# Kernel tuning notes

Measured on AMD Instinct MI355X. Metric: run time of the kernel, lower is better.

The kernel has to match this reference:

```python
import jax, jax.numpy as jnp
import numpy as np

NUM_EXPERTS = 8
TOP_K = 2
HIDDEN = 1024
INTER = 4096
B, S = 4, 2048


def setup_inputs() -> dict:
    key = jax.random.key(0)
    ks = jax.random.split(key, 5)
    scale_h = 1.0 / np.sqrt(HIDDEN)
    scale_f = 1.0 / np.sqrt(INTER)
    return {
        "hidden_states": jax.random.normal(ks[0], (B, S, HIDDEN), dtype=jnp.float32),
        "router_w": jax.random.normal(ks[1], (HIDDEN, NUM_EXPERTS), dtype=jnp.float32) * scale_h,
        "gate_w": jax.random.normal(ks[2], (NUM_EXPERTS, HIDDEN, INTER), dtype=jnp.float32) * scale_h,
        "up_w": jax.random.normal(ks[3], (NUM_EXPERTS, HIDDEN, INTER), dtype=jnp.float32) * scale_h,
        "down_w": jax.random.normal(ks[4], (NUM_EXPERTS, INTER, HIDDEN), dtype=jnp.float32) * scale_f,
    }


def reference(hidden_states, router_w, gate_w, up_w, down_w):
    # hidden_states: [B, S, D]
    Bsz, Sl, D = hidden_states.shape
    E = gate_w.shape[0]

    router_logits = jnp.einsum("bsd,de->bse", hidden_states, router_w)
    router_probs = jax.nn.softmax(router_logits, axis=-1)          # [B,S,E]
    expert_weights, expert_indices = jax.lax.top_k(router_probs, TOP_K)  # [B,S,K]
    expert_weights = expert_weights / jnp.sum(expert_weights, axis=-1, keepdims=True)

    # load-balance loss: usage_e = count(idx==e)/num_tokens (sums to K)
    num_tokens = Bsz * Sl
    one_hot = jax.nn.one_hot(expert_indices, E, dtype=router_probs.dtype)  # [B,S,K,E]
    expert_usage = jnp.sum(one_hot, axis=(0, 1, 2)) / num_tokens           # [E]
    mean_routing_prob = jnp.mean(router_probs, axis=(0, 1))                # [E]
    load_balance_loss = jnp.sum(expert_usage * mean_routing_prob) * E

    # combine weight per token per expert: [B,S,E]
    combine_w = jnp.einsum("bsk,bske->bse", expert_weights, one_hot)

    output = jnp.zeros_like(hidden_states)
    for e in range(E):  # small fixed expert count
        gate = jax.nn.silu(jnp.einsum("bsd,df->bsf", hidden_states, gate_w[e]))
        up = jnp.einsum("bsd,df->bsf", hidden_states, up_w[e])
        expert_out = jnp.einsum("bsf,fd->bsd", gate * up, down_w[e])
        output = output + combine_w[..., e, None] * expert_out

    return output, load_balance_loss
```

## Files before the change

### kernel.cpp

```cpp
#include <hip/hip_runtime.h>
#include <stdint.h>

#define T_TOK 8192
#define D_HID 1024
#define F_INT 4096
#define NEXP 8
#define NT2 (T_TOK*2)
#define BMR 256
#define NTIL 72
#define CBANKS 64

typedef __attribute__((ext_vector_type(4))) float f32x4;
typedef __attribute__((ext_vector_type(8))) __bf16 bf16x8;
typedef unsigned short u16;

__device__ __forceinline__ unsigned short f2bf(float x) {
  unsigned int u = __float_as_uint(x);
  u = u + 0x7FFFu + ((u >> 16) & 1u);
  return (unsigned short)(u >> 16);
}
__device__ __forceinline__ void gload_lds16(const void* g, void* l) {
  __builtin_amdgcn_global_load_lds(
      (const __attribute__((address_space(1))) unsigned int*)g,
      (__attribute__((address_space(3))) unsigned int*)l, 16, 0, 0);
}
__device__ __forceinline__ void wait_vm8() {
  asm volatile("s_waitcnt vmcnt(8)" ::: "memory");
  __builtin_amdgcn_sched_barrier(0);
}
__device__ __forceinline__ void wait_vm0() {
  asm volatile("s_waitcnt vmcnt(0)" ::: "memory");
  __builtin_amdgcn_sched_barrier(0);
}
__device__ __forceinline__ void wait_lgkm0() {
  asm volatile("s_waitcnt lgkmcnt(0)" ::: "memory");
  __builtin_amdgcn_sched_barrier(0);
}
__device__ __forceinline__ int tswz(int x) { return (x & 7) * 9 + (x >> 3); }

#define MFMA(a,b,c) __builtin_amdgcn_mfma_f32_16x16x32_bf16((a),(b),(c),0,0,0)

__global__ __launch_bounds__(256) void k_cvt_all(
    const float* __restrict__ gw, const float* __restrict__ uw,
    const float* __restrict__ dw,
    u16* __restrict__ gT, u16* __restrict__ uT, u16* __restrict__ dT) {
  int bx = blockIdx.x;
  int grp = bx >> 13;
  int idx = bx & 8191;
  int e = idx >> 10;
  int rem = idx & 1023;
  const float* in; u16* out; int R, C, cx, cy;
  if (grp == 0)      { in = gw; out = gT; R = D_HID; C = F_INT; cx = rem & 63; cy = rem >> 6; }
  else if (grp == 1) { in = uw; out = uT; R = D_HID; C = F_INT; cx = rem & 63; cy = rem >> 6; }
  else               { in = dw; out = dT; R = F_INT; C = D_HID; cx = rem & 15; cy = rem >> 4; }
  const size_t mat = (size_t)R * C;
  const float* ip = in + (size_t)e * mat;
  u16* op = out + (size_t)e * mat;
  int c0 = cx * 64, r0 = cy * 64;
  __shared__ float Tf[64][68];
  int t = threadIdx.x;
#pragma unroll
  for (int p = 0; p < 4; p++) {
    int r = p * 16 + (t >> 4);
    int c = (t & 15) * 4;
    float4 v = *(const float4*)(ip + (size_t)(r0 + r) * C + (c0 + c));
    *(float4*)&Tf[r][c] = v;
  }
  __syncthreads();
  int f = t >> 2, seg = (t & 3) * 16;
  union { u16 s[8]; uint4 q; } o0, o1;
#pragma unroll
  for (int j = 0; j < 8; j++) {
    o0.s[j] = f2bf(Tf[seg + j][f]);
    o1.s[j] = f2bf(Tf[seg + 8 + j][f]);
  }
  *(uint4*)(op + (size_t)(c0 + f) * R + r0 + seg) = o0.q;
  *(uint4*)(op + (size_t)(c0 + f) * R + r0 + seg + 8) = o1.q;
}

__global__ __launch_bounds__(256) void k_router(const float* __restrict__ h,
                                                const float* __restrict__ rw,
                                                u16* __restrict__ hb,
                                                int* __restrict__ cntB,
                                                float* __restrict__ psumB,
                                                int* __restrict__ topk_e,
                                                float* __restrict__ topk_w) {
  int t = blockIdx.x * 4 + (threadIdx.x >> 6);
  int l = threadIdx.x & 63;
  const float* hr = h + (size_t)t * D_HID;
  u16* hbr = hb + (size_t)t * D_HID;
  double acc[NEXP];
#pragma unroll
  for (int e = 0; e < NEXP; e++) acc[e] = 0.0;
#pragma unroll
  for (int it = 0; it < 4; it++) {
    int i = it * 256 + l * 4;
    float4 x4 = *(const float4*)(hr + i);
    union { u16 s[4]; uint2 q; } o;
    o.s[0] = f2bf(x4.x); o.s[1] = f2bf(x4.y); o.s[2] = f2bf(x4.z); o.s[3] = f2bf(x4.w);
    *(uint2*)(hbr + i) = o.q;
    const float* xp = &x4.x;
#pragma unroll
    for (int k = 0; k < 4; k++) {
      double x = (double)xp[k];
      const float4* r4 = (const float4*)(rw + (size_t)(i + k) * NEXP);
      float4 a = r4[0], b = r4[1];
      acc[0] += x * a.x; acc[1] += x * a.y; acc[2] += x * a.z; acc[3] += x * a.w;
      acc[4] += x * b.x; acc[5] += x * b.y; acc[6] += x * b.z; acc[7] += x * b.w;
    }
  }
#pragma unroll
  for (int m = 32; m >= 1; m >>= 1) {
#pragma unroll
    for (int e = 0; e < NEXP; e++) acc[e] += __shfl_xor(acc[e], m, 64);
  }
  if (l == 0) {
    double mx = acc[0];
#pragma unroll
    for (int e = 1; e < NEXP; e++) mx = fmax(mx, acc[e]);
    double p[NEXP], s = 0.0;
#pragma unroll
    for (int e = 0; e < NEXP; e++) { p[e] = exp(acc[e] - mx); s += p[e]; }
    int i0 = 0;
#pragma unroll
    for (int e = 1; e < NEXP; e++) if (p[e] > p[i0]) i0 = e;
    int i1 = (i0 == 0) ? 1 : 0;
#pragma unroll
    for (int e = 0; e < NEXP; e++) if (e != i0 && p[e] > p[i1]) i1 = e;
    double w0 = p[i0] / (p[i0] + p[i1]);
    topk_e[t] = i0 | (i1 << 8);
    topk_w[2 * t] = (float)w0;
    topk_w[2 * t + 1] = (float)(1.0 - w0);
    int bank = t & (CBANKS - 1);
    atomicAdd(&cntB[i0 * CBANKS + bank], 1);
    atomicAdd(&cntB[i1 * CBANKS + bank], 1);
    float inv = (float)(1.0 / s);
#pragma unroll
    for (int e = 0; e < NEXP; e++) atomicAdd(&psumB[e * CBANKS + bank], (float)p[e] * inv);
  }
}

__global__ void k_scan(const int* __restrict__ cntB, const float* __restrict__ psumB,
                       int* __restrict__ offs, int4* __restrict__ tiles,
                       int* __restrict__ meta, float* __restrict__ loss_out,
                       int* __restrict__ cnt2) {
  int l = threadIdx.x;
  int cs[NEXP]; float ps[NEXP];
#pragma unroll
  for (int e = 0; e < NEXP; e++) {
    int c = cntB[e * CBANKS + l];
    float p = psumB[e * CBANKS + l];
#pragma unroll
    for (int m = 32; m >= 1; m >>= 1) {
      c += __shfl_xor(c, m, 64);
      p += __shfl_xor(p, m, 64);
    }
    cs[e] = c; ps[e] = p;
  }
  if (l == 0) {
    int off = 0, tc = 0;
    double loss = 0.0;
    for (int e = 0; e < NEXP; e++) {
      loss += ((double)cs[e] / (double)T_TOK) * ((double)ps[e] / (double)T_TOK);
      offs[e] = off;
      int nt = (cs[e] + BMR - 1) / BMR;
      for (int j = 0; j < nt; j++) {
        int rem = cs[e] - j * BMR;
        tiles[tc] = make_int4(e, off + j * BMR, rem < BMR ? rem : BMR, 0);
        tc++;
      }
      off += cs[e];
      cnt2[e] = 0;
    }
    offs[NEXP] = off;
    meta[0] = tc;
    loss_out[0] = (float)(loss * (double)NEXP);
  }
}

__global__ __launch_bounds__(256) void k_scatter(const int* __restrict__ topk_e,
                                                 const float* __restrict__ topk_w,
                                                 const int* __restrict__ offs,
                                                 int* __restrict__ cnt2,
                                                 int* __restrict__ rowtok,
                                                 float* __restrict__ roww,
                                                 int* __restrict__ invmap) {
  int t = blockIdx.x * 256 + threadIdx.x;
  if (t >= T_TOK) return;
  int ee = topk_e[t];
#pragma unroll
  for (int k = 0; k < 2; k++) {
    int e = (ee >> (8 * k)) & 255;
    int pos = offs[e] + atomicAdd(&cnt2[e], 1);
    rowtok[pos] = t;
    roww[pos] = topk_w[2 * t + k];
    invmap[2 * t + k] = pos;
  }
}

__global__ __launch_bounds__(256) void k_combine(const float* __restrict__ P,
                                                 const int* __restrict__ invmap,
                                                 float* __restrict__ out) {
  int t = blockIdx.x;
  int d = threadIdx.x * 4;
  int pA = invmap[2 * t], pB = invmap[2 * t + 1];
  float4 a0 = *(const float4*)(P + (size_t)pA * D_HID + d);
  float4 a1 = *(const float4*)(P + ((size_t)NT2 + pA) * D_HID + d);
  float4 b0 = *(const float4*)(P + (size_t)pB * D_HID + d);
  float4 b1 = *(const float4*)(P + ((size_t)NT2 + pB) * D_HID + d);
  float4 r;
  r.x = (a0.x + a1.x) + (b0.x + b1.x);
  r.y = (a0.y + a1.y) + (b0.y + b1.y);
  r.z = (a0.z + a1.z) + (b0.z + b1.z);
  r.w = (a0.w + a1.w) + (b0.w + b1.w);
  *(float4*)(out + (size_t)t * D_HID + d) = r;
}

template <int MODE>
__global__ __launch_bounds__(512, 2) void k_mm8(
    const u16* __restrict__ Asrc, const u16* __restrict__ Bsrc,
    const u16* __restrict__ Bsrc2,
    const int4* __restrict__ tiles, const int* __restrict__ meta,
    const int* __restrict__ rowtok, const float* __restrict__ roww,
    u16* __restrict__ G, float* __restrict__ out,
    int fcb, int FC, int KLEN) {
  int bx, by;
  if constexpr (MODE == 3) {
    int s = ((int)blockIdx.x & 7) * 36 + ((int)blockIdx.x >> 3);
    bx = s >> 2; by = s & 3;
  } else {
    bx = tswz(blockIdx.x); by = blockIdx.y;
  }
  if (bx >= meta[0]) return;
  int4 td = tiles[bx];
  int eid = td.x, row0 = td.y, nrows = td.z;
  int kz = blockIdx.z;
  size_t kz_byte = (size_t)kz * KLEN * 2;

  __shared__ __align__(16) u16 lds[2][2][BMR][64];

  int tid = threadIdx.x;
  int l = tid & 63, wid = tid >> 6;
  int wr = wid >> 2, wc = wid & 3;

  int rr0 = wid * 8 + (l >> 3);
  int sw = ((l & 7) ^ (rr0 & 7)) << 4;
  const char* pA[4]; const char* pB[4];
#pragma unroll
  for (int j = 0; j < 4; j++) {
    int rr = j * 64 + rr0;
    if constexpr (MODE == 0) {
      int tok = rowtok[row0 + ((rr < nrows) ? rr : 0)];
      pA[j] = (const char*)Asrc + (size_t)tok * (D_HID * 2) + sw;
      const u16* wsrc = (j < 2) ? Bsrc : Bsrc2;
      int frow = fcb + by * 128 + (rr & 127);
      pB[j] = (const char*)wsrc + ((size_t)eid * F_INT + frow) * (D_HID * 2) + sw;
    } else {
      pA[j] = (const char*)Asrc + (size_t)(row0 + rr) * (FC * 2) + kz_byte + sw;
      int brow = by * 256 + rr;
      pB[j] = (const char*)Bsrc + ((size_t)eid * D_HID + brow) * (F_INT * 2) + kz_byte + sw;
    }
  }

  int ch0 = (((l >> 4) + 0) ^ (l & 7)) << 4;
  int ch1 = (((l >> 4) + 4) ^ (l & 7)) << 4;
  int offA = (wr * 128 + (l & 15)) * 128;
  int offBn[4];
#pragma unroll
  for (int n = 0; n < 4; n++) {
    int r;
    if constexpr (MODE == 0)
      r = (n < 2) ? (wc * 32 + n * 16) : (128 + wc * 32 + (n - 2) * 16);
    else
      r = wc * 64 + n * 16;
    offBn[n] = 32768 + (r + (l & 15)) * 128;
  }
  const char* base = (const char*)&lds[0][0][0][0];
#define LDA(b,m,s) (*(const bf16x8*)(base + (b)*65536 + offA + (m)*2048 + ((s)?ch1:ch0)))
#define LDB(b,n,s) (*(const bf16x8*)(base + (b)*65536 + offBn[n] + ((s)?ch1:ch0)))

  f32x4 acc[8][4];
#pragma unroll
  for (int m = 0; m < 8; m++)
#pragma unroll
    for (int n = 0; n < 4; n++) acc[m][n] = f32x4{0.f, 0.f, 0.f, 0.f};

  auto STAGE = [&](int b, int mat, const char* const* p, int kt) {
#pragma unroll
    for (int j = 0; j < 4; j++)
      gload_lds16(p[j] + (size_t)kt * 128, &lds[b][mat][j * 64 + wid * 8][0]);
  };

  auto TILE = [&](int b, int kts, bool dostage, int vm) {
    bf16x8 fa[4][2], fb[4][2];
#pragma unroll
    for (int m = 0; m < 4; m++) { fa[m][0] = LDA(b, m, 0); fa[m][1] = LDA(b, m, 1); }
#pragma unroll
    for (int n = 0; n < 2; n++) { fb[n][0] = LDB(b, n, 0); fb[n][1] = LDB(b, n, 1); }
    asm volatile("s_waitcnt lgkmcnt(8)" ::: "memory");
    __builtin_amdgcn_s_barrier();
    wait_lgkm0();
    __builtin_amdgcn_s_setprio(1);
#pragma unroll
    for (int m = 0; m < 4; m++)
#pragma unroll
      for (int n = 0; n < 2; n++) {
        acc[m][n] = MFMA(fa[m][0], fb[n][0], acc[m][n]);
        acc[m][n] = MFMA(fa[m][1], fb[n][1], acc[m][n]);
      }
    __builtin_amdgcn_s_setprio(0);
    __builtin_amdgcn_s_barrier();
#pragma unroll
    for (int n = 2; n < 4; n++) { fb[n][0] = LDB(b, n, 0); fb[n][1] = LDB(b, n, 1); }
    __builtin_amdgcn_s_barrier();
    wait_lgkm0();
    __builtin_amdgcn_s_setprio(1);
#pragma unroll
    for (int m = 0; m < 4; m++)
#pragma unroll
      for (int n = 2; n < 4; n++) {
        acc[m][n] = MFMA(fa[m][0], fb[n][0], acc[m][n]);
        acc[m][n] = MFMA(fa[m][1], fb[n][1], acc[m][n]);
      }
    __builtin_amdgcn_s_setprio(0);
    __builtin_amdgcn_s_barrier();
#pragma unroll
    for (int m = 0; m < 4; m++) { fa[m][0] = LDA(b, 4 + m, 0); fa[m][1] = LDA(b, 4 + m, 1); }
    if (dostage) STAGE(b, 1, pB, kts);
    __builtin_amdgcn_s_barrier();
    wait_lgkm0();
    __builtin_amdgcn_s_setprio(1);
#pragma unroll
    for (int m = 0; m < 4; m++)
#pragma unroll
      for (int n = 0; n < 2; n++) {
        acc[4 + m][n] = MFMA(fa[m][0], fb[n][0], acc[4 + m][n]);
        acc[4 + m][n] = MFMA(fa[m][1], fb[n][1], acc[4 + m][n]);
      }
    __builtin_amdgcn_s_setprio(0);
    __builtin_amdgcn_s_barrier();
    if (dostage) STAGE(b, 0, pA, kts);
    if (vm == 8) wait_vm8();
    else if (vm == 0) wait_vm0();
    __builtin_amdgcn_s_barrier();
    __builtin_amdgcn_s_setprio(1);
#pragma unroll
    for (int m = 0; m < 4; m++)
#pragma unroll
      for (int n = 2; n < 4; n++) {
        acc[4 + m][n] = MFMA(fa[m][0], fb[n][0], acc[4 + m][n]);
        acc[4 + m][n] = MFMA(fa[m][1], fb[n][1], acc[4 + m][n]);
      }
    __builtin_amdgcn_s_setprio(0);
    __builtin_amdgcn_s_barrier();
  };

  int NT = KLEN / 64;
  STAGE(0, 1, pB, 0); STAGE(0, 0, pA, 0);
  STAGE(1, 1, pB, 1); STAGE(1, 0, pA, 1);
  wait_vm8();
  __builtin_amdgcn_s_barrier();

  int NIT = NT / 2;
  for (int it = 0; it < NIT - 1; ++it) {
    TILE(0, 2 * it + 2, true, 8);
    TILE(1, 2 * it + 3, true, 8);
  }
  TILE(0, 0, false, 0);
  TILE(1, 0, false, -1);

  int lr = (l >> 4) * 4, lc = l & 15;
#pragma unroll
  for (int m = 0; m < 8; m++) {
    int rbase = wr * 128 + m * 16 + lr;
#pragma unroll
    for (int j = 0; j < 4; j++) {
      int r = rbase + j;
      if (r < nrows) {
        if constexpr (MODE == 0) {
          size_t gb = (size_t)(row0 + r) * FC + by * 128 + wc * 32 + lc;
#pragma unroll
          for (int n = 0; n < 2; n++) {
            float g = acc[m][n][j], u = acc[m][n + 2][j];
            float sv = g / (1.0f + __expf(-g));
            G[gb + n * 16] = f2bf(sv * u);
          }
        } else if constexpr (MODE == 2) {
          float w = roww[row0 + r];
          int tok = rowtok[row0 + r];
          size_t ob = (size_t)tok * D_HID + by * 256 + wc * 64 + lc;
#pragma unroll
          for (int n = 0; n < 4; n++) atomicAdd(&out[ob + n * 16], acc[m][n][j] * w);
        } else {
          float w = roww[row0 + r];
          size_t pb = ((size_t)kz * NT2 + (row0 + r)) * D_HID + by * 256 + wc * 64 + lc;
#pragma unroll
          for (int n = 0; n < 4; n++) out[pb + n * 16] = acc[m][n][j] * w;
        }
      }
    }
  }
#undef LDA
#undef LDB
}

extern "C" void kernel_launch(void* const* d_in, const int* in_sizes, int n_in,
                              void* d_out, int out_size, void* d_ws, size_t ws_size,
                              hipStream_t stream) {
  (void)in_sizes; (void)n_in;
  const float* h  = (const float*)d_in[0];
  const float* rw = (const float*)d_in[1];
  const float* gw = (const float*)d_in[2];
  const float* uw = (const float*)d_in[3];
  const float* dw = (const float*)d_in[4];
  float* out = (float*)d_out;

  char* base = (char*)d_ws;
  size_t off = 0;
  auto alloc = [&](size_t b) -> char* {
    char* r = base + off;
    off += (b + 255) & ~(size_t)255;
    return r;
  };

  u16*   hb     = (u16*)alloc((size_t)T_TOK * D_HID * 2);
  int*   cntB   = (int*)alloc(NEXP * CBANKS * 4);
  float* psumB  = (float*)alloc(NEXP * CBANKS * 4);
  int*   offs   = (int*)alloc((NEXP + 1) * 4);
  int*   cnt2   = (int*)alloc(NEXP * 4);
  int*   meta   = (int*)alloc(64);
  int4*  tiles  = (int4*)alloc(NTIL * sizeof(int4));
  int*   topk_e = (int*)alloc(T_TOK * 4);
  float* topk_w = (float*)alloc((size_t)T_TOK * 2 * 4);
  int*   rowtok = (int*)alloc(NT2 * 4);
  float* roww   = (float*)alloc(NT2 * 4);
  int*   invmap = (int*)alloc(NT2 * 4);

  size_t zbytes = (size_t)((char*)topk_e - (char*)cntB);

  const size_t GROWS = NT2 + (size_t)BMR * NEXP;
  const size_t EDF = (size_t)NEXP * D_HID * F_INT;
  size_t avail = (ws_size > off) ? ws_size - off : 0;
  auto need = [&](int nc) -> size_t {
    return 3 * EDF * 2 + GROWS * (size_t)(F_INT / nc) * 2 + 65536;
  };
  int nchunk = 4;
  if      (avail >= need(1)) nchunk = 1;
  else if (avail >= need(2)) nchunk = 2;
  u16* gT = (u16*)alloc(EDF * 2);
  u16* uT = (u16*)alloc(EDF * 2);
  u16* dT = (u16*)alloc(EDF * 2);
  int FC = F_INT / nchunk;
  u16* G = (u16*)alloc(GROWS * (size_t)FC * 2);

  hipMemsetAsync(cntB, 0, zbytes, stream);
  if (nchunk != 1) hipMemsetAsync(d_out, 0, (size_t)out_size * 4, stream);

  k_router<<<T_TOK / 4, 256, 0, stream>>>(h, rw, hb, cntB, psumB, topk_e, topk_w);
  k_scan<<<1, 64, 0, stream>>>(cntB, psumB, offs, tiles, meta, out + (out_size - 1), cnt2);
  k_scatter<<<T_TOK / 256, 256, 0, stream>>>(topk_e, topk_w, offs, cnt2, rowtok, roww, invmap);
  k_cvt_all<<<24576, 256, 0, stream>>>(gw, uw, dw, gT, uT, dT);

  if (nchunk == 1) {
    float* P = (float*)gT;
    dim3 g1(NTIL, F_INT / 128, 1);
    dim3 g2(NTIL * 4, 1, 2);
    k_mm8<0><<<g1, 512, 0, stream>>>(hb, gT, uT, tiles, meta, rowtok, roww, G, out,
                                     0, F_INT, D_HID);
    k_mm8<3><<<g2, 512, 0, stream>>>(G, dT, dT, tiles, meta, rowtok, roww, G, P,
                                     0, F_INT, F_INT / 2);
    k_combine<<<T_TOK, 256, 0, stream>>>(P, invmap, out);
  } else {
    for (int c = 0; c < nchunk; c++) {
      int fcb = c * FC;
      dim3 g1(NTIL, FC / 128, 1);
      dim3 g2(NTIL, D_HID / 256, 2);
      k_mm8<0><<<g1, 512, 0, stream>>>(hb, gT, uT, tiles, meta, rowtok, roww, G, out,
                                       fcb, FC, D_HID);
      k_mm8<2><<<g2, 512, 0, stream>>>(G, dT, dT, tiles, meta, rowtok, roww, G, out,
                                       fcb, FC, FC / 2);
    }
  }
}
```

Measured before the change: 802.2 us.

## Halve down-projection row tile to 128 for finer grid and simpler pipeline

Adds a second tile list with 128-row tiles per expert and uses it for the MODE 3 down-projection GEMM, giving each block 4 M-fragments instead of 8 and roughly doubling the number of blocks. The MODE 3 inner loop drops the split A-fragment phases and stages A (2 loads) and B together with a vmcnt(6) wait. The aim is better CU fill and less tail/padding waste in the down GEMM, at the cost of more B-weight reloads per output and lower arithmetic intensity per block.

After: 806.9 us. About the same (+0.6%).

```diff
diff --git a/kernel.cpp b/kernel.cpp
--- a/kernel.cpp
+++ b/kernel.cpp
@@ -8,6 +8,7 @@
 #define NT2 (T_TOK*2)
 #define BMR 256
 #define NTIL 72
+#define NTIL2 136
 #define CBANKS 64
 
 typedef __attribute__((ext_vector_type(4))) float f32x4;
@@ -26,6 +27,10 @@
 }
 __device__ __forceinline__ void wait_vm8() {
   asm volatile("s_waitcnt vmcnt(8)" ::: "memory");
+  __builtin_amdgcn_sched_barrier(0);
+}
+__device__ __forceinline__ void wait_vm6() {
+  asm volatile("s_waitcnt vmcnt(6)" ::: "memory");
   __builtin_amdgcn_sched_barrier(0);
 }
 __device__ __forceinline__ void wait_vm0() {
@@ -142,6 +147,7 @@
 
 __global__ void k_scan(const int* __restrict__ cntB, const float* __restrict__ psumB,
                        int* __restrict__ offs, int4* __restrict__ tiles,
+                       int4* __restrict__ tiles2,
                        int* __restrict__ meta, float* __restrict__ loss_out,
                        int* __restrict__ cnt2) {
   int l = threadIdx.x;
@@ -158,7 +164,7 @@
     cs[e] = c; ps[e] = p;
   }
   if (l == 0) {
-    int off = 0, tc = 0;
+    int off = 0, tc = 0, t2 = 0;
     double loss = 0.0;
     for (int e = 0; e < NEXP; e++) {
       loss += ((double)cs[e] / (double)T_TOK) * ((double)ps[e] / (double)T_TOK);
@@ -169,11 +175,18 @@
         tiles[tc] = make_int4(e, off + j * BMR, rem < BMR ? rem : BMR, 0);
         tc++;
       }
+      int nt2 = (cs[e] + 127) / 128;
+      for (int j = 0; j < nt2; j++) {
+        int rem = cs[e] - j * 128;
+        tiles2[t2] = make_int4(e, off + j * 128, rem < 128 ? rem : 128, 0);
+        t2++;
+      }
       off += cs[e];
       cnt2[e] = 0;
     }
     offs[NEXP] = off;
     meta[0] = tc;
+    meta[1] = t2;
     loss_out[0] = (float)(loss * (double)NEXP);
   }
 }
@@ -224,14 +237,16 @@
     const int* __restrict__ rowtok, const float* __restrict__ roww,
     u16* __restrict__ G, float* __restrict__ out,
     int fcb, int FC, int KLEN) {
+  constexpr int MR = (MODE == 3) ? 4 : 8;
   int bx, by;
   if constexpr (MODE == 3) {
-    int s = ((int)blockIdx.x & 7) * 36 + ((int)blockIdx.x >> 3);
+    int s = ((int)blockIdx.x & 7) * 68 + ((int)blockIdx.x >> 3);
     bx = s >> 2; by = s & 3;
+    if (bx >= meta[1]) return;
   } else {
     bx = tswz(blockIdx.x); by = blockIdx.y;
-  }
-  if (bx >= meta[0]) return;
+    if (bx >= meta[0]) return;
+  }
   int4 td = tiles[bx];
   int eid = td.x, row0 = td.y, nrows = td.z;
   int kz = blockIdx.z;
@@ -249,6 +264,7 @@
 #pragma unroll
   for (int j = 0; j < 4; j++) {
     int rr = j * 64 + rr0;
+    int rrA = ((MODE == 3) ? (j & 1) : j) * 64 + rr0;
     if constexpr (MODE == 0) {
       int tok = rowtok[row0 + ((rr < nrows) ? rr : 0)];
       pA[j] = (const char*)Asrc + (size_t)tok * (D_HID * 2) + sw;
@@ -256,7 +272,7 @@
       int frow = fcb + by * 128 + (rr & 127);
       pB[j] = (const char*)wsrc + ((size_t)eid * F_INT + frow) * (D_HID * 2) + sw;
     } else {
-      pA[j] = (const char*)Asrc + (size_t)(row0 + rr) * (FC * 2) + kz_byte + sw;
+      pA[j] = (const char*)Asrc + (size_t)(row0 + rrA) * (FC * 2) + kz_byte + sw;
       int brow = by * 256 + rr;
       pB[j] = (const char*)Bsrc + ((size_t)eid * D_HID + brow) * (F_INT * 2) + kz_byte + sw;
     }
@@ -264,7 +280,7 @@
 
   int ch0 = (((l >> 4) + 0) ^ (l & 7)) << 4;
   int ch1 = (((l >> 4) + 4) ^ (l & 7)) << 4;
-  int offA = (wr * 128 + (l & 15)) * 128;
+  int offA = ((MODE == 3 ? wr * 64 : wr * 128) + (l & 15)) * 128;
   int offBn[4];
 #pragma unroll
   for (int n = 0; n < 4; n++) {
@@ -279,16 +295,21 @@
 #define LDA(b,m,s) (*(const bf16x8*)(base + (b)*65536 + offA + (m)*2048 + ((s)?ch1:ch0)))
 #define LDB(b,n,s) (*(const bf16x8*)(base + (b)*65536 + offBn[n] + ((s)?ch1:ch0)))
 
-  f32x4 acc[8][4];
-#pragma unroll
-  for (int m = 0; m < 8; m++)
+  f32x4 acc[MR][4];
+#pragma unroll
+  for (int m = 0; m < MR; m++)
 #pragma unroll
     for (int n = 0; n < 4; n++) acc[m][n] = f32x4{0.f, 0.f, 0.f, 0.f};
 
-  auto STAGE = [&](int b, int mat, const char* const* p, int kt) {
+  auto STAGE_B = [&](int b, int kt) {
 #pragma unroll
     for (int j = 0; j < 4; j++)
-      gload_lds16(p[j] + (size_t)kt * 128, &lds[b][mat][j * 64 + wid * 8][0]);
+      gload_lds16(pB[j] + (size_t)kt * 128, &lds[b][1][j * 64 + wid * 8][0]);
+  };
+  auto STAGE_A = [&](int b, int kt) {
+#pragma unroll
+    for (int j = 0; j < ((MODE == 3) ? 2 : 4); j++)
+      gload_lds16(pA[j] + (size_t)kt * 128, &lds[b][0][j * 64 + wid * 8][0]);
   };
 
   auto TILE = [&](int b, int kts, bool dostage, int vm) {
@@ -324,55 +345,63 @@
       }
     __builtin_amdgcn_s_setprio(0);
     __builtin_amdgcn_s_barrier();
-#pragma unroll
-    for (int m = 0; m < 4; m++) { fa[m][0] = LDA(b, 4 + m, 0); fa[m][1] = LDA(b, 4 + m, 1); }
-    if (dostage) STAGE(b, 1, pB, kts);
-    __builtin_amdgcn_s_barrier();
-    wait_lgkm0();
-    __builtin_amdgcn_s_setprio(1);
-#pragma unroll
-    for (int m = 0; m < 4; m++)
-#pragma unroll
-      for (int n = 0; n < 2; n++) {
-        acc[4 + m][n] = MFMA(fa[m][0], fb[n][0], acc[4 + m][n]);
-        acc[4 + m][n] = MFMA(fa[m][1], fb[n][1], acc[4 + m][n]);
-      }
-    __builtin_amdgcn_s_setprio(0);
-    __builtin_amdgcn_s_barrier();
-    if (dostage) STAGE(b, 0, pA, kts);
-    if (vm == 8) wait_vm8();
-    else if (vm == 0) wait_vm0();
-    __builtin_amdgcn_s_barrier();
-    __builtin_amdgcn_s_setprio(1);
-#pragma unroll
-    for (int m = 0; m < 4; m++)
-#pragma unroll
-      for (int n = 2; n < 4; n++) {
-        acc[4 + m][n] = MFMA(fa[m][0], fb[n][0], acc[4 + m][n]);
-        acc[4 + m][n] = MFMA(fa[m][1], fb[n][1], acc[4 + m][n]);
-      }
-    __builtin_amdgcn_s_setprio(0);
-    __builtin_amdgcn_s_barrier();
+    if constexpr (MODE == 3) {
+      if (dostage) { STAGE_B(b, kts); STAGE_A(b, kts); }
+      if (vm == 6) wait_vm6();
+      else if (vm == 0) wait_vm0();
+      __builtin_amdgcn_s_barrier();
+    } else {
+#pragma unroll
+      for (int m = 0; m < 4; m++) { fa[m][0] = LDA(b, 4 + m, 0); fa[m][1] = LDA(b, 4 + m, 1); }
+      if (dostage) STAGE_B(b, kts);
+      __builtin_amdgcn_s_barrier();
+      wait_lgkm0();
+      __builtin_amdgcn_s_setprio(1);
+#pragma unroll
+      for (int m = 0; m < 4; m++)
+#pragma unroll
+        for (int n = 0; n < 2; n++) {
+          acc[(MR - 4) + m][n] = MFMA(fa[m][0], fb[n][0], acc[(MR - 4) + m][n]);
+          acc[(MR - 4) + m][n] = MFMA(fa[m][1], fb[n][1], acc[(MR - 4) + m][n]);
+        }
+      __builtin_amdgcn_s_setprio(0);
+      __builtin_amdgcn_s_barrier();
+      if (dostage) STAGE_A(b, kts);
+      if (vm == 8) wait_vm8();
+      else if (vm == 0) wait_vm0();
+      __builtin_amdgcn_s_barrier();
+      __builtin_amdgcn_s_setprio(1);
+#pragma unroll
+      for (int m = 0; m < 4; m++)
+#pragma unroll
+        for (int n = 2; n < 4; n++) {
+          acc[(MR - 4) + m][n] = MFMA(fa[m][0], fb[n][0], acc[(MR - 4) + m][n]);
+          acc[(MR - 4) + m][n] = MFMA(fa[m][1], fb[n][1], acc[(MR - 4) + m][n]);
+        }
+      __builtin_amdgcn_s_setprio(0);
+      __builtin_amdgcn_s_barrier();
+    }
   };
 
   int NT = KLEN / 64;
-  STAGE(0, 1, pB, 0); STAGE(0, 0, pA, 0);
-  STAGE(1, 1, pB, 1); STAGE(1, 0, pA, 1);
-  wait_vm8();
+  int VMN = (MODE == 3) ? 6 : 8;
+  STAGE_B(0, 0); STAGE_A(0, 0);
+  STAGE_B(1, 1); STAGE_A(1, 1);
+  if constexpr (MODE == 3) wait_vm6(); else wait_vm8();
   __builtin_amdgcn_s_barrier();
 
   int NIT = NT / 2;
   for (int it = 0; it < NIT - 1; ++it) {
-    TILE(0, 2 * it + 2, true, 8);
-    TILE(1, 2 * it + 3, true, 8);
+    TILE(0, 2 * it + 2, true, VMN);
+    TILE(1, 2 * it + 3, true, VMN);
   }
   TILE(0, 0, false, 0);
   TILE(1, 0, false, -1);
 
   int lr = (l >> 4) * 4, lc = l & 15;
 #pragma unroll
-  for (int m = 0; m < 8; m++) {
-    int rbase = wr * 128 + m * 16 + lr;
+  for (int m = 0; m < MR; m++) {
+    int rbase = (MODE == 3 ? wr * 64 : wr * 128) + m * 16 + lr;
 #pragma unroll
     for (int j = 0; j < 4; j++) {
       int r = rbase + j;
@@ -430,6 +459,7 @@
   int*   cnt2   = (int*)alloc(NEXP * 4);
   int*   meta   = (int*)alloc(64);
   int4*  tiles  = (int4*)alloc(NTIL * sizeof(int4));
+  int4*  tiles2 = (int4*)alloc(NTIL2 * sizeof(int4));
   int*   topk_e = (int*)alloc(T_TOK * 4);
   float* topk_w = (float*)alloc((size_t)T_TOK * 2 * 4);
   int*   rowtok = (int*)alloc(NT2 * 4);
@@ -457,17 +487,18 @@
   if (nchunk != 1) hipMemsetAsync(d_out, 0, (size_t)out_size * 4, stream);
 
   k_router<<<T_TOK / 4, 256, 0, stream>>>(h, rw, hb, cntB, psumB, topk_e, topk_w);
-  k_scan<<<1, 64, 0, stream>>>(cntB, psumB, offs, tiles, meta, out + (out_size - 1), cnt2);
+  k_scan<<<1, 64, 0, stream>>>(cntB, psumB, offs, tiles, tiles2, meta,
+                               out + (out_size - 1), cnt2);
   k_scatter<<<T_TOK / 256, 256, 0, stream>>>(topk_e, topk_w, offs, cnt2, rowtok, roww, invmap);
   k_cvt_all<<<24576, 256, 0, stream>>>(gw, uw, dw, gT, uT, dT);
 
   if (nchunk == 1) {
     float* P = (float*)gT;
     dim3 g1(NTIL, F_INT / 128, 1);
-    dim3 g2(NTIL * 4, 1, 2);
+    dim3 g2(NTIL2 * 4, 1, 2);
     k_mm8<0><<<g1, 512, 0, stream>>>(hb, gT, uT, tiles, meta, rowtok, roww, G, out,
                                      0, F_INT, D_HID);
-    k_mm8<3><<<g2, 512, 0, stream>>>(G, dT, dT, tiles, meta, rowtok, roww, G, P,
+    k_mm8<3><<<g2, 512, 0, stream>>>(G, dT, dT, tiles2, meta, rowtok, roww, G, P,
                                      0, F_INT, F_INT / 2);
     k_combine<<<T_TOK, 256, 0, stream>>>(P, invmap, out);
   } else {
```
